# Optimization experiments

Hardware: AMD Instinct MI355X
Metric: run time of the kernel (lower is better)

The kernel has to match this reference:

```python
import jax, jax.numpy as jnp
import numpy as np

B, S, D = 2, 2048, 1024
H, DK = 16, 64


def setup_inputs() -> dict:
    key = jax.random.key(0)
    ks = jax.random.split(key, 5)
    x = jax.random.normal(ks[0], (B, S, D), dtype=jnp.float32)
    attn_w = jax.random.normal(ks[1], (3 * H * DK, D), dtype=jnp.float32) * (1.0 / np.sqrt(D))
    attn_b = jax.random.normal(ks[2], (3 * H * DK,), dtype=jnp.float32) * 0.02
    proj_w = jax.random.normal(ks[3], (D, H * DK), dtype=jnp.float32) * (1.0 / np.sqrt(H * DK))
    proj_b = jax.random.normal(ks[4], (D,), dtype=jnp.float32) * 0.02
    return {"x": x, "attn_w": attn_w, "attn_b": attn_b, "proj_w": proj_w, "proj_b": proj_b}


def reference(x, attn_w, attn_b, proj_w, proj_b):
    b, s, d = x.shape
    # fused QKV projection (torch Linear: x @ W.T + b)
    qkv = x @ attn_w.T + attn_b  # [b, s, 3*H*DK]
    q, k, v = jnp.split(qkv, 3, axis=2)
    # [b, s, H, DK] -> [b, H, s, DK]
    q = q.reshape(b, s, H, DK).transpose(0, 2, 1, 3)
    k = k.reshape(b, s, H, DK).transpose(0, 2, 1, 3)
    v = v.reshape(b, s, H, DK).transpose(0, 2, 1, 3)
    scale = 1.0 / np.sqrt(DK).astype(np.float32)
    scores = jnp.einsum('bhqd,bhkd->bhqk', q, k) * scale  # [b, H, s, s]
    causal = jnp.tril(jnp.ones((s, s), dtype=bool))
    scores = jnp.where(causal, scores, jnp.finfo(scores.dtype).min)
    attn = jax.nn.softmax(scores, axis=-1)
    out = jnp.einsum('bhqk,bhkd->bhqd', attn, v)  # [b, H, s, DK]
    out = out.transpose(0, 2, 1, 3).reshape(b, s, H * DK)
    return out @ proj_w.T + proj_b
```

## Files before the change

kernel.cpp:

```cpp
#include <hip/hip_runtime.h>
#include <hip/hip_bf16.h>
#include <stdint.h>


typedef __bf16 bf16_t;
typedef __bf16 bf16x8 __attribute__((ext_vector_type(8)));
typedef float f32x4 __attribute__((ext_vector_type(4)));

#define B_SZ 2
#define S_LEN 2048
#define D_MODEL 1024
#define N_HEADS 16
#define D_HEAD 64
#define M_ROWS (B_SZ * S_LEN)
#define QKV_N (3 * N_HEADS * D_HEAD)

#define Q_SCALE 0.1803368801111204f

#define OFF_XB  (0ull)
#define OFF_WB  (8ull  << 20)
#define OFF_PWB (14ull << 20)
#define OFF_Q   (16ull << 20)
#define OFF_K   (24ull << 20)
#define OFF_VT  (32ull << 20)
#define OFF_AO  (40ull << 20)

__device__ __forceinline__ unsigned short f2bf_u(float f) {
  union { float f; unsigned u; } v; v.f = f;
  unsigned r = v.u + 0x7fffu + ((v.u >> 16) & 1u);
  return (unsigned short)(r >> 16);
}
__device__ __forceinline__ bf16_t f2bf(float f) {
  unsigned short u = f2bf_u(f);
  return __builtin_bit_cast(bf16_t, u);
}
__device__ __forceinline__ unsigned cvt_pk_bf16(float lo, float hi) {
  unsigned r;
  asm volatile("v_cvt_pk_bf16_f32 %0, %1, %2" : "=v"(r) : "v"(lo), "v"(hi));
  return r;
}

__global__ void cvt3_f32_bf16(const float* __restrict__ sa, bf16_t* __restrict__ da, int n4a,
                              const float* __restrict__ sb, bf16_t* __restrict__ db, int n4b,
                              const float* __restrict__ sc, bf16_t* __restrict__ dc, int n4c) {
  int i = blockIdx.x * blockDim.x + threadIdx.x;
  const float* s; bf16_t* d; int j = i;
  if (i < n4a) { s = sa; d = da; }
  else if ((j = i - n4a) < n4b) { s = sb; d = db; }
  else if ((j = i - n4a - n4b) < n4c) { s = sc; d = dc; }
  else return;
  float4 f = reinterpret_cast<const float4*>(s)[j];
  ushort4 o;
  o.x = f2bf_u(f.x); o.y = f2bf_u(f.y); o.z = f2bf_u(f.z); o.w = f2bf_u(f.w);
  reinterpret_cast<ushort4*>(d)[j] = o;
}

#define BM 128
#define BN 128
#define BK 64

__device__ __forceinline__ void gload_lds16(const bf16_t* g, bf16_t* l) {
  __builtin_amdgcn_global_load_lds((__attribute__((address_space(1))) void*)g,
                                   (__attribute__((address_space(3))) void*)l,
                                   16, 0, 0);
}

__device__ __forceinline__ bf16x8 lds_frag(const bf16_t* lds, int row, int kchunk) {
  int pos = kchunk ^ (row & 7);
  return *reinterpret_cast<const bf16x8*>(lds + row * BK + pos * 8);
}

template <int EPI>
__global__ __launch_bounds__(256, 3) void gemm_bt(
    const bf16_t* __restrict__ A, const bf16_t* __restrict__ Bt,
    const float* __restrict__ bias,
    float* __restrict__ fout,
    bf16_t* __restrict__ qout, bf16_t* __restrict__ kout,
    bf16_t* __restrict__ vtout,
    int M, int N, int K) {
  __shared__ bf16_t As[BM * BK];
  __shared__ bf16_t Bs[BN * BK];
  const int tid = threadIdx.x;
  const int lane = tid & 63;
  const int wid = tid >> 6;
  const int wr = wid >> 1, wc = wid & 1;
  const int cl = lane & 15, hl = lane >> 4;

  const int id = blockIdx.x;
  const int xcd = id & 7, loc = id >> 3;
  int mtile, ntile;
  if constexpr (EPI == 0) {
    mtile = (xcd & 3) * 8 + (loc & 7);
    ntile = (xcd >> 2) * 12 + (loc >> 3);
  } else {
    mtile = xcd * 4 + (loc & 3);
    ntile = loc >> 2;
  }
  const int m0 = mtile * BM, n0 = ntile * BN;

  f32x4 acc[4][4];
  #pragma unroll
  for (int m = 0; m < 4; ++m)
    #pragma unroll
    for (int n = 0; n < 4; ++n)
      acc[m][n] = (f32x4){0.f, 0.f, 0.f, 0.f};

  for (int kt = 0; kt < K; kt += BK) {
    #pragma unroll
    for (int it = 0; it < 4; ++it) {
      int chunk = it * 256 + tid;
      int row = chunk >> 3, cpos = chunk & 7;
      int csrc = cpos ^ (row & 7);
      bf16_t* ldsA = As + (it * 256 + wid * 64) * 8;
      bf16_t* ldsB = Bs + (it * 256 + wid * 64) * 8;
      gload_lds16(A  + (size_t)(m0 + row) * K + kt + csrc * 8, ldsA);
      gload_lds16(Bt + (size_t)(n0 + row) * K + kt + csrc * 8, ldsB);
    }
    __syncthreads();

    bf16x8 af[2][4], bfr[2][4];
    #pragma unroll
    for (int kk = 0; kk < 2; ++kk) {
      #pragma unroll
      for (int m = 0; m < 4; ++m)
        af[kk][m] = lds_frag(As, wr * 64 + m * 16 + cl, kk * 4 + hl);
      #pragma unroll
      for (int n = 0; n < 4; ++n)
        bfr[kk][n] = lds_frag(Bs, wc * 64 + n * 16 + cl, kk * 4 + hl);
    }
    __builtin_amdgcn_s_setprio(1);
    #pragma unroll
    for (int m = 0; m < 4; ++m)
      #pragma unroll
      for (int n = 0; n < 4; ++n) {
        acc[m][n] = __builtin_amdgcn_mfma_f32_16x16x32_bf16(af[0][m], bfr[0][n], acc[m][n], 0, 0, 0);
        acc[m][n] = __builtin_amdgcn_mfma_f32_16x16x32_bf16(af[1][m], bfr[1][n], acc[m][n], 0, 0, 0);
      }
    __builtin_amdgcn_s_setprio(0);
    __syncthreads();
  }

  #pragma unroll
  for (int n = 0; n < 4; ++n) {
    int ng = n0 + wc * 64 + n * 16 + cl;
    float bv = bias[ng];
    if constexpr (EPI == 0) {
      int part = ng >> 10;
      int r = ng & 1023;
      int h = r >> 6, dk = r & 63;
      #pragma unroll
      for (int m = 0; m < 4; ++m)
        #pragma unroll
        for (int j = 0; j < 4; ++j) {
          int mg = m0 + wr * 64 + m * 16 + hl * 4 + j;
          int b = mg >> 11, s = mg & 2047;
          float val = acc[m][n][j] + bv;
          size_t bh = (size_t)(b * N_HEADS + h);
          if (part == 0)
            qout[(bh * S_LEN + s) * D_HEAD + dk] = f2bf(val * Q_SCALE);
          else if (part == 1)
            kout[(bh * S_LEN + s) * D_HEAD + dk] = f2bf(val);
          else
            vtout[(bh * D_HEAD + dk) * S_LEN + s] = f2bf(val);
        }
    } else {
      #pragma unroll
      for (int m = 0; m < 4; ++m)
        #pragma unroll
        for (int j = 0; j < 4; ++j) {
          int mg = m0 + wr * 64 + m * 16 + hl * 4 + j;
          fout[(size_t)mg * N + ng] = acc[m][n][j] + bv;
        }
    }
  }
}

__global__ __launch_bounds__(512, 2) void attn_fwd(
    const bf16_t* __restrict__ q,
    const bf16_t* __restrict__ k,
    const bf16_t* __restrict__ vt,
    bf16_t* __restrict__ ao) {
  const int blk = blockIdx.x;
  const int half = blk >> 8;
  const int low = blk & 255;
  const int bh = (low & 7) * 4 + ((low >> 3) & 3);
  const int qp = low >> 5;
  const int qt = half ? (15 - qp) : qp;
  const int tid = threadIdx.x;
  const int lane = tid & 63, w = tid >> 6;
  const int cl = lane & 15, hl = lane >> 4;
  const bf16_t* qb = q + (size_t)bh * S_LEN * D_HEAD;
  const bf16_t* kb = k + (size_t)bh * S_LEN * D_HEAD;
  const bf16_t* vb = vt + (size_t)bh * D_HEAD * S_LEN;
  const int b = bh >> 4, h = bh & 15;

  __shared__ bf16_t kvbuf[2][2][4096];
  __shared__ bf16_t plds[8][16][72];

  const int srow = tid >> 3;
  const int scc = (tid & 7) ^ (srow & 7);
  const int sw = cl & 7;

  const int row0 = qt * 128 + w * 16;
  const int ktb = 2 * qt + 1;

  const bf16_t* qr = qb + (size_t)(row0 + cl) * D_HEAD + hl * 8;
  bf16x8 qf0 = *reinterpret_cast<const bf16x8*>(qr);
  bf16x8 qf1 = *reinterpret_cast<const bf16x8*>(qr + 32);

  float mrow = -1e30f, lrow = 0.f;
  f32x4 acco[4];
  #pragma unroll
  for (int db = 0; db < 4; ++db) acco[db] = (f32x4){0.f, 0.f, 0.f, 0.f};

  gload_lds16(kb + (size_t)srow * D_HEAD + scc * 8, &kvbuf[0][0][w << 9]);
  gload_lds16(vb + (size_t)srow * S_LEN + scc * 8,  &kvbuf[0][1][w << 9]);
  __syncthreads();

  int cur = 0;
  for (int kt = 0; kt <= ktb; ++kt) {
    if (kt < ktb) {
      gload_lds16(kb + (size_t)((kt + 1) * 64 + srow) * D_HEAD + scc * 8,
                  &kvbuf[cur ^ 1][0][w << 9]);
      gload_lds16(vb + (size_t)srow * S_LEN + (kt + 1) * 64 + scc * 8,
                  &kvbuf[cur ^ 1][1][w << 9]);
    }

    const bool act = (kt * 64) <= (row0 + 15);
    if (act) {
      const bf16_t* kB = kvbuf[cur][0];
      const bf16_t* vB = kvbuf[cur][1];
      bf16x8 kf[4][2], vf[4][2];
      #pragma unroll
      for (int nb = 0; nb < 4; ++nb) {
        const bf16_t* kr = kB + (nb * 16 + cl) * 64;
        kf[nb][0] = *reinterpret_cast<const bf16x8*>(kr + ((hl ^ sw) << 3));
        kf[nb][1] = *reinterpret_cast<const bf16x8*>(kr + (((hl + 4) ^ sw) << 3));
      }
      #pragma unroll
      for (int db = 0; db < 4; ++db) {
        const bf16_t* vr = vB + (db * 16 + cl) * 64;
        vf[db][0] = *reinterpret_cast<const bf16x8*>(vr + ((hl ^ sw) << 3));
        vf[db][1] = *reinterpret_cast<const bf16x8*>(vr + (((hl + 4) ^ sw) << 3));
      }

      f32x4 sacc[4];
      __builtin_amdgcn_s_setprio(1);
      #pragma unroll
      for (int nb = 0; nb < 4; ++nb) {
        f32x4 s = (f32x4){0.f, 0.f, 0.f, 0.f};
        s = __builtin_amdgcn_mfma_f32_16x16x32_bf16(kf[nb][0], qf0, s, 0, 0, 0);
        s = __builtin_amdgcn_mfma_f32_16x16x32_bf16(kf[nb][1], qf1, s, 0, 0, 0);
        sacc[nb] = s;
      }
      __builtin_amdgcn_s_setprio(0);

      const int qrow = row0 + cl;
      if (kt * 64 + 63 > qrow) {
        #pragma unroll
        for (int nb = 0; nb < 4; ++nb)
          #pragma unroll
          for (int jj = 0; jj < 4; ++jj) {
            int kpos = kt * 64 + nb * 16 + hl * 4 + jj;
            if (kpos > qrow) sacc[nb][jj] = -1e30f;
          }
      }
      float tm = sacc[0][0];
      #pragma unroll
      for (int nb = 0; nb < 4; ++nb)
        #pragma unroll
        for (int jj = 0; jj < 4; ++jj)
          tm = fmaxf(tm, sacc[nb][jj]);
      tm = fmaxf(tm, __shfl_xor(tm, 16));
      tm = fmaxf(tm, __shfl_xor(tm, 32));
      if (__any(tm > mrow + 8.f)) {
        float mnew = fmaxf(mrow, tm);
        float corr = __builtin_amdgcn_exp2f(mrow - mnew);
        mrow = mnew;
        lrow *= corr;
        #pragma unroll
        for (int db = 0; db < 4; ++db) acco[db] *= corr;
      }
      float rs = 0.f;
      #pragma unroll
      for (int nb = 0; nb < 4; ++nb)
        #pragma unroll
        for (int jj = 0; jj < 4; ++jj) {
          float p = __builtin_amdgcn_exp2f(sacc[nb][jj] - mrow);
          sacc[nb][jj] = p;
          rs += p;
        }
      rs += __shfl_xor(rs, 16);
      rs += __shfl_xor(rs, 32);
      lrow += rs;
      #pragma unroll
      for (int nb = 0; nb < 4; ++nb) {
        uint2 u;
        u.x = cvt_pk_bf16(sacc[nb][0], sacc[nb][1]);
        u.y = cvt_pk_bf16(sacc[nb][2], sacc[nb][3]);
        *reinterpret_cast<uint2*>(&plds[w][cl][nb * 16 + hl * 4]) = u;
      }

      bf16x8 pf0 = *reinterpret_cast<const bf16x8*>(&plds[w][cl][hl * 8]);
      bf16x8 pf1 = *reinterpret_cast<const bf16x8*>(&plds[w][cl][32 + hl * 8]);
      __builtin_amdgcn_s_setprio(1);
      #pragma unroll
      for (int db = 0; db < 4; ++db) {
        acco[db] = __builtin_amdgcn_mfma_f32_16x16x32_bf16(vf[db][0], pf0, acco[db], 0, 0, 0);
        acco[db] = __builtin_amdgcn_mfma_f32_16x16x32_bf16(vf[db][1], pf1, acco[db], 0, 0, 0);
      }
      __builtin_amdgcn_s_setprio(0);
    }

    __syncthreads();
    cur ^= 1;
  }

  {
    float linv = 1.f / lrow;
    const int qrow = row0 + cl;
    #pragma unroll
    for (int db = 0; db < 4; ++db) {
      uint2 u;
      u.x = cvt_pk_bf16(acco[db][0] * linv, acco[db][1] * linv);
      u.y = cvt_pk_bf16(acco[db][2] * linv, acco[db][3] * linv);
      *reinterpret_cast<uint2*>(
          ao + ((size_t)(b * S_LEN) + qrow) * D_MODEL + h * D_HEAD + db * 16 + hl * 4) = u;
    }
  }
}

extern "C" void kernel_launch(void* const* d_in, const int* in_sizes, int n_in,
                              void* d_out, int out_size, void* d_ws, size_t ws_size,
                              hipStream_t stream) {
  const float* x      = (const float*)d_in[0];
  const float* attn_w = (const float*)d_in[1];
  const float* attn_b = (const float*)d_in[2];
  const float* proj_w = (const float*)d_in[3];
  const float* proj_b = (const float*)d_in[4];
  float* out = (float*)d_out;
  char* ws = (char*)d_ws;

  bf16_t* xb  = (bf16_t*)(ws + OFF_XB);
  bf16_t* wb  = (bf16_t*)(ws + OFF_WB);
  bf16_t* pwb = (bf16_t*)(ws + OFF_PWB);
  bf16_t* qb  = (bf16_t*)(ws + OFF_Q);
  bf16_t* kb  = (bf16_t*)(ws + OFF_K);
  bf16_t* vtb = (bf16_t*)(ws + OFF_VT);
  bf16_t* aob = (bf16_t*)(ws + OFF_AO);

  const int n4a = M_ROWS * D_MODEL / 4;
  const int n4b = QKV_N * D_MODEL / 4;
  const int n4c = D_MODEL * D_MODEL / 4;
  const int n4 = n4a + n4b + n4c;
  cvt3_f32_bf16<<<(n4 + 255) / 256, 256, 0, stream>>>(x, xb, n4a, attn_w, wb, n4b,
                                                      proj_w, pwb, n4c);

  gemm_bt<0><<<dim3(768), 256, 0, stream>>>(
      xb, wb, attn_b, nullptr, qb, kb, vtb, M_ROWS, QKV_N, D_MODEL);

  attn_fwd<<<dim3(512), 512, 0, stream>>>(qb, kb, vtb, aob);

  gemm_bt<1><<<dim3(256), 256, 0, stream>>>(
      aob, pwb, proj_b, out, nullptr, nullptr, nullptr, M_ROWS, D_MODEL, D_MODEL);
}
```

Baseline: 116.9 us.

## Stage GEMM epilogues through LDS for coalesced vector stores

Replaces the scattered per-element bf16/f32 stores in the GEMM epilogues with staging through shared memory, then wide row-contiguous 16-byte stores. For Q/K, tiles are written to a padded LDS buffer and copied out as contiguous 64-element head rows. The V^T part uses packed 8-byte stores along the sequence dimension. The projection output goes through a padded f32 LDS tile in two passes. This adds LDS traffic and extra barriers, and grows shared memory to 34 KB, which may reduce occupancy.

```diff
diff --git a/kernel.cpp b/kernel.cpp
--- a/kernel.cpp
+++ b/kernel.cpp
@@ -78,8 +78,10 @@
     bf16_t* __restrict__ qout, bf16_t* __restrict__ kout,
     bf16_t* __restrict__ vtout,
     int M, int N, int K) {
-  __shared__ bf16_t As[BM * BK];
-  __shared__ bf16_t Bs[BN * BK];
+  __shared__ __align__(16) char smem[34816];
+  bf16_t* As = reinterpret_cast<bf16_t*>(smem);
+  bf16_t* Bs = As + BM * BK;
+
   const int tid = threadIdx.x;
   const int lane = tid & 63;
   const int wid = tid >> 6;
@@ -140,37 +142,84 @@
     __syncthreads();
   }
 
-  #pragma unroll
-  for (int n = 0; n < 4; ++n) {
-    int ng = n0 + wc * 64 + n * 16 + cl;
-    float bv = bias[ng];
-    if constexpr (EPI == 0) {
-      int part = ng >> 10;
-      int r = ng & 1023;
-      int h = r >> 6, dk = r & 63;
-      #pragma unroll
-      for (int m = 0; m < 4; ++m)
-        #pragma unroll
-        for (int j = 0; j < 4; ++j) {
-          int mg = m0 + wr * 64 + m * 16 + hl * 4 + j;
-          int b = mg >> 11, s = mg & 2047;
-          float val = acc[m][n][j] + bv;
-          size_t bh = (size_t)(b * N_HEADS + h);
-          if (part == 0)
-            qout[(bh * S_LEN + s) * D_HEAD + dk] = f2bf(val * Q_SCALE);
-          else if (part == 1)
-            kout[(bh * S_LEN + s) * D_HEAD + dk] = f2bf(val);
-          else
-            vtout[(bh * D_HEAD + dk) * S_LEN + s] = f2bf(val);
+  if constexpr (EPI == 0) {
+    const int part = n0 >> 10;
+    const int b = m0 >> 11;
+    const int sloc = m0 & 2047;
+    if (part == 2) {
+      #pragma unroll
+      for (int n = 0; n < 4; ++n) {
+        int ng = n0 + wc * 64 + n * 16 + cl;
+        float bv = bias[ng];
+        int r = ng & 1023;
+        int h = r >> 6, dk = r & 63;
+        bf16_t* vrow = vtout + ((size_t)((b * N_HEADS + h) * D_HEAD + dk)) * S_LEN;
+        #pragma unroll
+        for (int m = 0; m < 4; ++m) {
+          int sbase = sloc + wr * 64 + m * 16 + hl * 4;
+          uint2 u;
+          u.x = cvt_pk_bf16(acc[m][n][0] + bv, acc[m][n][1] + bv);
+          u.y = cvt_pk_bf16(acc[m][n][2] + bv, acc[m][n][3] + bv);
+          *reinterpret_cast<uint2*>(vrow + sbase) = u;
         }
+      }
     } else {
-      #pragma unroll
-      for (int m = 0; m < 4; ++m)
-        #pragma unroll
-        for (int j = 0; j < 4; ++j) {
-          int mg = m0 + wr * 64 + m * 16 + hl * 4 + j;
-          fout[(size_t)mg * N + ng] = acc[m][n][j] + bv;
+      const float scale = (part == 0) ? Q_SCALE : 1.0f;
+      bf16_t (*ct)[136] = reinterpret_cast<bf16_t(*)[136]>(smem);
+      #pragma unroll
+      for (int n = 0; n < 4; ++n) {
+        int colb = wc * 64 + n * 16 + cl;
+        float bv = bias[n0 + colb];
+        #pragma unroll
+        for (int m = 0; m < 4; ++m)
+          #pragma unroll
+          for (int j = 0; j < 4; ++j) {
+            int row = wr * 64 + m * 16 + hl * 4 + j;
+            ct[row][colb] = f2bf((acc[m][n][j] + bv) * scale);
+          }
+      }
+      __syncthreads();
+      bf16_t* dst = (part == 0) ? qout : kout;
+      const int row = tid >> 1, seg = tid & 1;
+      const int ngs = n0 + seg * 64;
+      const int h = (ngs & 1023) >> 6;
+      const int s = sloc + row;
+      bf16_t* drow = dst + ((size_t)((b * N_HEADS + h) * S_LEN + s)) * D_HEAD;
+      #pragma unroll
+      for (int kk = 0; kk < 8; ++kk) {
+        uint4 v = *reinterpret_cast<const uint4*>(&ct[row][seg * 64 + kk * 8]);
+        *reinterpret_cast<uint4*>(drow + kk * 8) = v;
+      }
+    }
+  } else {
+    float (*ctf)[68] = reinterpret_cast<float(*)[68]>(smem);
+    #pragma unroll 1
+    for (int p = 0; p < 2; ++p) {
+      if (wc == p) {
+        #pragma unroll
+        for (int n = 0; n < 4; ++n) {
+          int coll = n * 16 + cl;
+          float bv = bias[n0 + p * 64 + coll];
+          #pragma unroll
+          for (int m = 0; m < 4; ++m)
+            #pragma unroll
+            for (int j = 0; j < 4; ++j) {
+              int row = wr * 64 + m * 16 + hl * 4 + j;
+              ctf[row][coll] = acc[m][n][j] + bv;
+            }
         }
+      }
+      __syncthreads();
+      {
+        const int row = tid >> 1, sub = tid & 1;
+        float* drow = fout + (size_t)(m0 + row) * N + n0 + p * 64 + sub * 32;
+        #pragma unroll
+        for (int kk = 0; kk < 8; ++kk) {
+          float4 v = *reinterpret_cast<const float4*>(&ctf[row][sub * 32 + kk * 4]);
+          *reinterpret_cast<float4*>(drow + kk * 4) = v;
+        }
+      }
+      __syncthreads();
     }
   }
 }
```

New measurement: 116.4 us, median of 4. About the same (-0.4%).
